# Kernel optimization log

Measured on AMD Instinct MI355X. Metric: run time of the kernel, lower is better.

Reference implementation:

```python
import jax, jax.numpy as jnp
import numpy as np

N_NODES = 50000
N_EDGES = 800000
IN_FEATS = 256
HIDDEN = 128
OUT_FEATS = 64


def setup_inputs() -> dict:
    key = jax.random.key(0)
    k1, k2, k3, k4, k5 = jax.random.split(key, 5)
    x = jax.random.normal(k1, (N_NODES, IN_FEATS), dtype=jnp.float32)
    src = jax.random.randint(k2, (N_EDGES,), 0, N_NODES, dtype=jnp.int64)
    dst = jax.random.randint(k3, (N_EDGES,), 0, N_NODES, dtype=jnp.int64)
    # Glorot-ish init for linear weights (DGL GraphConv uses xavier_uniform)
    W1 = jax.random.normal(k4, (IN_FEATS, HIDDEN), dtype=jnp.float32) / np.sqrt(IN_FEATS)
    W2 = jax.random.normal(k5, (HIDDEN, OUT_FEATS), dtype=jnp.float32) / np.sqrt(HIDDEN)
    b1 = jnp.zeros((HIDDEN,), dtype=jnp.float32)
    b2 = jnp.zeros((OUT_FEATS,), dtype=jnp.float32)
    return {"x": x, "src": src, "dst": dst, "W1": W1, "b1": b1, "W2": W2, "b2": b2}


def _norms(src, dst, n_nodes):
    ones = jnp.ones(src.shape[0], dtype=jnp.float32)
    deg_out = jax.ops.segment_sum(ones, src, num_segments=n_nodes)
    deg_in = jax.ops.segment_sum(ones, dst, num_segments=n_nodes)
    # DGL clamps zero degrees to 1 to avoid inf
    norm_src = jnp.power(jnp.clip(deg_out, 1.0, None), -0.5)  # [N]
    norm_dst = jnp.power(jnp.clip(deg_in, 1.0, None), -0.5)   # [N]
    return norm_src, norm_dst


def _gcn_layer(h, W, b, src, dst, norm_src, norm_dst, n_nodes):
    # norm='both': D_dst^{-1/2} A D_src^{-1/2} (h W) + b
    # multiply by W first (in_feats >= out_feats -> cheaper aggregation)
    m = (h * norm_src[:, None]) @ W            # [N, out]
    agg = jax.ops.segment_sum(m[src], dst, num_segments=n_nodes)  # [N, out]
    return agg * norm_dst[:, None] + b


def reference(x, src, dst, W1, b1, W2, b2):
    n = x.shape[0]
    norm_src, norm_dst = _norms(src, dst, n)
    h = _gcn_layer(x, W1, b1, src, dst, norm_src, norm_dst, n)
    h = jax.nn.relu(h)
    h = _gcn_layer(h, W2, b2, src, dst, norm_src, norm_dst, n)
    return h
```

## Files before the change

kernel.cpp:

```cpp
#include <hip/hip_runtime.h>

#define N_NODES 50000
#define N_EDGES 800000
#define IN_FEATS 256
#define HIDDEN 128
#define OUT_FEATS 64

#define NB 16384
#define NRANGE 4
#define NBT (NRANGE * NB)
#define NCHUNK 64
#define EPC 12500

typedef _Float16 f16;
typedef _Float16 f16x8 __attribute__((ext_vector_type(8)));
typedef float f32x4 __attribute__((ext_vector_type(4)));

__global__ __launch_bounds__(256) void hist_kernel(
    const int* __restrict__ src, const int* __restrict__ dst,
    unsigned* __restrict__ hist_src, unsigned* __restrict__ hist_dst) {
  __shared__ unsigned ls[NB / 2];
  __shared__ unsigned ld2[NB / 2];
  const int r = blockIdx.x % NRANGE;
  const int c = blockIdx.x / NRANGE;
  const int lo = r * NB;
  for (int i = threadIdx.x; i < NB / 2; i += 256) {
    ls[i] = 0;
    ld2[i] = 0;
  }
  __syncthreads();
  const int4* s4 = (const int4*)(src + c * EPC);
  const int4* d4 = (const int4*)(dst + c * EPC);
  for (int i = threadIdx.x; i < EPC / 4; i += 256) {
    int4 s = s4[i];
    int4 d = d4[i];
    unsigned b;
    b = (unsigned)(s.x - lo); if (b < NB) atomicAdd(&ls[b >> 1], 1u << ((b & 1) << 4));
    b = (unsigned)(s.y - lo); if (b < NB) atomicAdd(&ls[b >> 1], 1u << ((b & 1) << 4));
    b = (unsigned)(s.z - lo); if (b < NB) atomicAdd(&ls[b >> 1], 1u << ((b & 1) << 4));
    b = (unsigned)(s.w - lo); if (b < NB) atomicAdd(&ls[b >> 1], 1u << ((b & 1) << 4));
    b = (unsigned)(d.x - lo); if (b < NB) atomicAdd(&ld2[b >> 1], 1u << ((b & 1) << 4));
    b = (unsigned)(d.y - lo); if (b < NB) atomicAdd(&ld2[b >> 1], 1u << ((b & 1) << 4));
    b = (unsigned)(d.z - lo); if (b < NB) atomicAdd(&ld2[b >> 1], 1u << ((b & 1) << 4));
    b = (unsigned)(d.w - lo); if (b < NB) atomicAdd(&ld2[b >> 1], 1u << ((b & 1) << 4));
  }
  __syncthreads();
  unsigned* hs = hist_src + ((long)c * NBT + lo) / 2;
  unsigned* hd = hist_dst + ((long)c * NBT + lo) / 2;
  for (int i = threadIdx.x; i < NB / 2; i += 256) {
    hs[i] = ls[i];
    hd[i] = ld2[i];
  }
}

__global__ __launch_bounds__(256) void reduce_kernel(
    const unsigned* __restrict__ hist_src, unsigned* __restrict__ hist_dst,
    int* __restrict__ deg_in, float* __restrict__ norm_src,
    float* __restrict__ norm_dst, int* __restrict__ partial) {
  const unsigned short* hs = (const unsigned short*)hist_src;
  unsigned short* hd = (unsigned short*)hist_dst;
  int n = blockIdx.x * 256 + threadIdx.x;
  int run = 0;
  if (n < N_NODES) {
    int so = 0;
#pragma unroll 8
    for (int c = 0; c < NCHUNK; ++c) so += hs[(long)c * NBT + n];
    norm_src[n] = rsqrtf((float)max(so, 1));
#pragma unroll 8
    for (int c = 0; c < NCHUNK; ++c) {
      int t = hd[(long)c * NBT + n];
      hd[(long)c * NBT + n] = (unsigned short)run;
      run += t;
    }
    deg_in[n] = run;
    norm_dst[n] = rsqrtf((float)max(run, 1));
  }
  __shared__ int sd[256];
  sd[threadIdx.x] = run;
  __syncthreads();
  for (int s = 128; s > 0; s >>= 1) {
    if (threadIdx.x < s) sd[threadIdx.x] += sd[threadIdx.x + s];
    __syncthreads();
  }
  if (threadIdx.x == 0) partial[blockIdx.x] = sd[0];
}

__global__ __launch_bounds__(256) void scan2(int* __restrict__ partial,
                                             int nb) {
  __shared__ int sd[256];
  int v = (threadIdx.x < nb) ? partial[threadIdx.x] : 0;
  sd[threadIdx.x] = v;
  __syncthreads();
  for (int off = 1; off < 256; off <<= 1) {
    int t = sd[threadIdx.x] +
            ((threadIdx.x >= off) ? sd[threadIdx.x - off] : 0);
    __syncthreads();
    sd[threadIdx.x] = t;
    __syncthreads();
  }
  if (threadIdx.x < nb) partial[threadIdx.x] = sd[threadIdx.x] - v;
}

__global__ __launch_bounds__(256) void scan3(const int* __restrict__ deg,
                                             const int* __restrict__ partial,
                                             int* __restrict__ rowptr) {
  __shared__ int sd[256];
  int i = blockIdx.x * 256 + threadIdx.x;
  int v = (i < N_NODES) ? deg[i] : 0;
  sd[threadIdx.x] = v;
  __syncthreads();
  for (int off = 1; off < 256; off <<= 1) {
    int t = sd[threadIdx.x] +
            ((threadIdx.x >= off) ? sd[threadIdx.x - off] : 0);
    __syncthreads();
    sd[threadIdx.x] = t;
    __syncthreads();
  }
  if (i < N_NODES) rowptr[i] = partial[blockIdx.x] + sd[threadIdx.x] - v;
  if (blockIdx.x == 0 && threadIdx.x == 0) rowptr[N_NODES] = N_EDGES;
}

__global__ __launch_bounds__(256) void fill_csr(
    const int* __restrict__ src, const int* __restrict__ dst,
    const int* __restrict__ rowptr, const unsigned* __restrict__ pref32,
    int* __restrict__ col) {
  __shared__ int cur[NB];
  const unsigned short* pref = (const unsigned short*)pref32;
  const int r = blockIdx.x % NRANGE;
  const int c = blockIdx.x / NRANGE;
  const int lo = r * NB;
  for (int i = threadIdx.x; i < NB; i += 256) {
    int n = lo + i;
    cur[i] = (n < N_NODES) ? rowptr[n] + pref[(long)c * NBT + n] : 0;
  }
  __syncthreads();
  const int4* s4 = (const int4*)(src + c * EPC);
  const int4* d4 = (const int4*)(dst + c * EPC);
  for (int i = threadIdx.x; i < EPC / 4; i += 256) {
    int4 s = s4[i];
    int4 d = d4[i];
    unsigned b;
    b = (unsigned)(d.x - lo);
    if (b < NB) col[atomicAdd(&cur[b], 1)] = s.x;
    b = (unsigned)(d.y - lo);
    if (b < NB) col[atomicAdd(&cur[b], 1)] = s.y;
    b = (unsigned)(d.z - lo);
    if (b < NB) col[atomicAdd(&cur[b], 1)] = s.z;
    b = (unsigned)(d.w - lo);
    if (b < NB) col[atomicAdd(&cur[b], 1)] = s.w;
  }
}

__global__ __launch_bounds__(256) void wtrans(const float* __restrict__ W1,
                                              const float* __restrict__ W2,
                                              f16* __restrict__ W1T,
                                              f16* __restrict__ W2T) {
  int i = blockIdx.x * 256 + threadIdx.x;
  if (i < 128 * 256) {
    int n = i >> 8, k = i & 255;
    W1T[i] = (f16)W1[k * 128 + n];
  } else if (i < 128 * 256 + 64 * 128) {
    int j = i - 128 * 256;
    int n = j >> 7, k = j & 127;
    W2T[j] = (f16)W2[k * 64 + n];
  }
}

template <int K, int NC, int TN, bool FP32IN>
__global__ __launch_bounds__(256) void gemm_mfma(
    const void* __restrict__ Xv, const f16* __restrict__ WT,
    const float* __restrict__ ns, f16* __restrict__ Mout) {
  constexpr int KI = K / 32;
  constexpr int COLBLK = NC / (TN * 16);
  constexpr int KP = K + 8;
  __shared__ f16 Bs[TN * 16 * KP];

  const int cb = blockIdx.x % COLBLK;
  const int rb = blockIdx.x / COLBLK;
  const int col0 = cb * TN * 16;
  const int wave = threadIdx.x >> 6;
  const int lane = threadIdx.x & 63;
  const int m = lane & 15;
  const int q = lane >> 4;
  const int row0 = rb * 64 + wave * 16;

  for (int idx = threadIdx.x; idx < TN * 16 * (K / 8); idx += 256) {
    int n = idx / (K / 8);
    int kk = idx % (K / 8);
    *(f16x8*)(Bs + n * KP + kk * 8) =
        *(const f16x8*)(WT + (long)(col0 + n) * K + kk * 8);
  }
  __syncthreads();

  const int ra = min(row0 + m, N_NODES - 1);
  const float s = FP32IN ? ns[ra] : 0.f;

  f32x4 acc[TN];
#pragma unroll
  for (int t = 0; t < TN; ++t) acc[t] = (f32x4){0.f, 0.f, 0.f, 0.f};

#pragma unroll
  for (int ki = 0; ki < KI; ++ki) {
    const int kb = ki * 32 + q * 8;
    f16x8 a;
    if (FP32IN) {
      const float* X = (const float*)Xv;
      const float* p = X + (long)ra * K + kb;
      float4 u0 = *(const float4*)p;
      float4 u1 = *(const float4*)(p + 4);
      a[0] = (f16)(u0.x * s); a[1] = (f16)(u0.y * s);
      a[2] = (f16)(u0.z * s); a[3] = (f16)(u0.w * s);
      a[4] = (f16)(u1.x * s); a[5] = (f16)(u1.y * s);
      a[6] = (f16)(u1.z * s); a[7] = (f16)(u1.w * s);
    } else {
      const f16* X = (const f16*)Xv;
      a = *(const f16x8*)(X + (long)ra * K + kb);
    }
#pragma unroll
    for (int t = 0; t < TN; ++t) {
      f16x8 b = *(const f16x8*)(Bs + (t * 16 + m) * KP + kb);
      acc[t] = __builtin_amdgcn_mfma_f32_16x16x32_f16(a, b, acc[t], 0, 0, 0);
    }
  }

#pragma unroll
  for (int r = 0; r < 4; ++r) {
    int row = row0 + q * 4 + r;
    if (row < N_NODES) {
#pragma unroll
      for (int t = 0; t < TN; ++t)
        Mout[(long)row * NC + col0 + t * 16 + m] = (f16)acc[t][r];
    }
  }
}

__global__ __launch_bounds__(256) void gather1_kernel(
    const f16* __restrict__ M, const int* __restrict__ rowptr,
    const int* __restrict__ col, const float* __restrict__ nd,
    const float* __restrict__ ns, const float* __restrict__ b,
    f16* __restrict__ out) {
  constexpr int LPR = 16;
  constexpr int EPW = 64 / LPR;
  const int wave = threadIdx.x >> 6;
  const int lane = threadIdx.x & 63;
  const int eg = lane / LPR;
  const int t = lane % LPR;
  const int n = blockIdx.x * 4 + wave;
  if (n >= N_NODES) return;
  const int beg = rowptr[n];
  const int end = rowptr[n + 1];

  float acc[8];
#pragma unroll
  for (int j = 0; j < 8; ++j) acc[j] = 0.f;

  int i = beg + eg;
  for (; i + EPW < end; i += 2 * EPW) {
    int s0 = col[i];
    int s1 = col[i + EPW];
    f16x8 v0 = *(const f16x8*)(M + (long)s0 * HIDDEN + t * 8);
    f16x8 v1 = *(const f16x8*)(M + (long)s1 * HIDDEN + t * 8);
#pragma unroll
    for (int j = 0; j < 8; ++j) acc[j] += (float)v0[j] + (float)v1[j];
  }
  if (i < end) {
    int s0 = col[i];
    f16x8 v0 = *(const f16x8*)(M + (long)s0 * HIDDEN + t * 8);
#pragma unroll
    for (int j = 0; j < 8; ++j) acc[j] += (float)v0[j];
  }

#pragma unroll
  for (int m2 = LPR; m2 < 64; m2 <<= 1)
#pragma unroll
    for (int j = 0; j < 8; ++j) acc[j] += __shfl_xor(acc[j], m2, 64);

  if (eg == 0) {
    float s = nd[n];
    float sn = ns[n];
    float4 bb0 = *(const float4*)(b + t * 8);
    float4 bb1 = *(const float4*)(b + t * 8 + 4);
    f16x8 o;
    o[0] = (f16)(fmaxf(acc[0] * s + bb0.x, 0.f) * sn);
    o[1] = (f16)(fmaxf(acc[1] * s + bb0.y, 0.f) * sn);
    o[2] = (f16)(fmaxf(acc[2] * s + bb0.z, 0.f) * sn);
    o[3] = (f16)(fmaxf(acc[3] * s + bb0.w, 0.f) * sn);
    o[4] = (f16)(fmaxf(acc[4] * s + bb1.x, 0.f) * sn);
    o[5] = (f16)(fmaxf(acc[5] * s + bb1.y, 0.f) * sn);
    o[6] = (f16)(fmaxf(acc[6] * s + bb1.z, 0.f) * sn);
    o[7] = (f16)(fmaxf(acc[7] * s + bb1.w, 0.f) * sn);
    *(f16x8*)(out + (long)n * HIDDEN + t * 8) = o;
  }
}

__global__ __launch_bounds__(256) void gather2_kernel(
    const f16* __restrict__ M, const int* __restrict__ rowptr,
    const int* __restrict__ col, const float* __restrict__ nd,
    const float* __restrict__ b, float* __restrict__ out) {
  constexpr int LPR = 8;
  constexpr int EPW = 64 / LPR;
  const int wave = threadIdx.x >> 6;
  const int lane = threadIdx.x & 63;
  const int eg = lane / LPR;
  const int t = lane % LPR;
  const int n = blockIdx.x * 4 + wave;
  if (n >= N_NODES) return;
  const int beg = rowptr[n];
  const int end = rowptr[n + 1];

  float acc[8];
#pragma unroll
  for (int j = 0; j < 8; ++j) acc[j] = 0.f;

  int i = beg + eg;
  for (; i + EPW < end; i += 2 * EPW) {
    int s0 = col[i];
    int s1 = col[i + EPW];
    f16x8 v0 = *(const f16x8*)(M + (long)s0 * OUT_FEATS + t * 8);
    f16x8 v1 = *(const f16x8*)(M + (long)s1 * OUT_FEATS + t * 8);
#pragma unroll
    for (int j = 0; j < 8; ++j) acc[j] += (float)v0[j] + (float)v1[j];
  }
  if (i < end) {
    int s0 = col[i];
    f16x8 v0 = *(const f16x8*)(M + (long)s0 * OUT_FEATS + t * 8);
#pragma unroll
    for (int j = 0; j < 8; ++j) acc[j] += (float)v0[j];
  }

#pragma unroll
  for (int m2 = LPR; m2 < 64; m2 <<= 1)
#pragma unroll
    for (int j = 0; j < 8; ++j) acc[j] += __shfl_xor(acc[j], m2, 64);

  if (eg == 0) {
    float s = nd[n];
    float4 bb0 = *(const float4*)(b + t * 8);
    float4 bb1 = *(const float4*)(b + t * 8 + 4);
    float4 o0, o1;
    o0.x = acc[0] * s + bb0.x;
    o0.y = acc[1] * s + bb0.y;
    o0.z = acc[2] * s + bb0.z;
    o0.w = acc[3] * s + bb0.w;
    o1.x = acc[4] * s + bb1.x;
    o1.y = acc[5] * s + bb1.y;
    o1.z = acc[6] * s + bb1.z;
    o1.w = acc[7] * s + bb1.w;
    *(float4*)(out + (long)n * OUT_FEATS + t * 8) = o0;
    *(float4*)(out + (long)n * OUT_FEATS + t * 8 + 4) = o1;
  }
}

extern "C" void kernel_launch(void* const* d_in, const int* in_sizes, int n_in,
                              void* d_out, int out_size, void* d_ws,
                              size_t ws_size, hipStream_t stream) {
  const float* x = (const float*)d_in[0];
  const int* src = (const int*)d_in[1];
  const int* dst = (const int*)d_in[2];
  const float* W1 = (const float*)d_in[3];
  const float* b1 = (const float*)d_in[4];
  const float* W2 = (const float*)d_in[5];
  const float* b2 = (const float*)d_in[6];
  float* out = (float*)d_out;

  int* wi = (int*)d_ws;
  int* partial = wi;
  int* rowptr = wi + 256;
  int* deg_in = wi + 50260;
  int* col = wi + 100260;
  float* wf = (float*)d_ws + 900260;
  float* norm_src = wf;
  float* norm_dst = wf + 50000;
  f16* fh = (f16*)(wf + 100000);
  f16* W1T = fh;
  f16* W2T = fh + 128 * 256;
  f16* m1 = fh + 128 * 256 + 64 * 128;
  f16* h1p = m1 + (long)50048 * 128;
  f16* m2 = h1p + (long)50048 * 128;

  unsigned* hist_src = (unsigned*)m1;
  unsigned* hist_dst = hist_src + (long)NCHUNK * NBT / 2;

  const int nb_nodes = (N_NODES + 255) / 256;
  const int rowblk = (N_NODES + 63) / 64;

  hist_kernel<<<NRANGE * NCHUNK, 256, 0, stream>>>(src, dst, hist_src,
                                                   hist_dst);
  reduce_kernel<<<nb_nodes, 256, 0, stream>>>(hist_src, hist_dst, deg_in,
                                              norm_src, norm_dst, partial);
  scan2<<<1, 256, 0, stream>>>(partial, nb_nodes);
  scan3<<<nb_nodes, 256, 0, stream>>>(deg_in, partial, rowptr);
  fill_csr<<<NRANGE * NCHUNK, 256, 0, stream>>>(src, dst, rowptr, hist_dst,
                                                col);
  wtrans<<<(128 * 256 + 64 * 128 + 255) / 256, 256, 0, stream>>>(W1, W2, W1T,
                                                                 W2T);

  gemm_mfma<IN_FEATS, HIDDEN, 4, true>
      <<<rowblk * 2, 256, 0, stream>>>(x, W1T, norm_src, m1);
  gather1_kernel<<<(N_NODES + 3) / 4, 256, 0, stream>>>(m1, rowptr, col,
                                                        norm_dst, norm_src, b1,
                                                        h1p);

  gemm_mfma<HIDDEN, OUT_FEATS, 4, false>
      <<<rowblk, 256, 0, stream>>>(h1p, W2T, norm_src, m2);
  gather2_kernel<<<(N_NODES + 3) / 4, 256, 0, stream>>>(m2, rowptr, col,
                                                        norm_dst, b2, out);
}
```

Before: 241.5 us.

## Fuse CSR-building prep kernels into one cooperative kernel with grid syncs

Merges the histogram, degree reduction, two scan stages, CSR fill and weight transpose into a single cooperative kernel of 256 blocks separated by grid-wide barriers. This removes five kernel launches and their inter-kernel gaps from the preprocessing chain. In exchange, later phases run on a fixed 256-block grid with loops over work items, and each grid.sync adds barrier cost. The 64KB shared array may limit occupancy but must fit for the cooperative launch to succeed.

```diff
diff --git a/kernel.cpp b/kernel.cpp
--- a/kernel.cpp
+++ b/kernel.cpp
@@ -1,4 +1,7 @@
 #include <hip/hip_runtime.h>
+#include <hip/hip_cooperative_groups.h>
+
+namespace cg = cooperative_groups;
 
 #define N_NODES 50000
 #define N_EDGES 800000
@@ -16,153 +19,163 @@
 typedef _Float16 f16x8 __attribute__((ext_vector_type(8)));
 typedef float f32x4 __attribute__((ext_vector_type(4)));
 
-__global__ __launch_bounds__(256) void hist_kernel(
+__global__ __launch_bounds__(256) void prep_kernel(
     const int* __restrict__ src, const int* __restrict__ dst,
-    unsigned* __restrict__ hist_src, unsigned* __restrict__ hist_dst) {
-  __shared__ unsigned ls[NB / 2];
-  __shared__ unsigned ld2[NB / 2];
-  const int r = blockIdx.x % NRANGE;
-  const int c = blockIdx.x / NRANGE;
-  const int lo = r * NB;
-  for (int i = threadIdx.x; i < NB / 2; i += 256) {
-    ls[i] = 0;
-    ld2[i] = 0;
-  }
-  __syncthreads();
-  const int4* s4 = (const int4*)(src + c * EPC);
-  const int4* d4 = (const int4*)(dst + c * EPC);
-  for (int i = threadIdx.x; i < EPC / 4; i += 256) {
-    int4 s = s4[i];
-    int4 d = d4[i];
-    unsigned b;
-    b = (unsigned)(s.x - lo); if (b < NB) atomicAdd(&ls[b >> 1], 1u << ((b & 1) << 4));
-    b = (unsigned)(s.y - lo); if (b < NB) atomicAdd(&ls[b >> 1], 1u << ((b & 1) << 4));
-    b = (unsigned)(s.z - lo); if (b < NB) atomicAdd(&ls[b >> 1], 1u << ((b & 1) << 4));
-    b = (unsigned)(s.w - lo); if (b < NB) atomicAdd(&ls[b >> 1], 1u << ((b & 1) << 4));
-    b = (unsigned)(d.x - lo); if (b < NB) atomicAdd(&ld2[b >> 1], 1u << ((b & 1) << 4));
-    b = (unsigned)(d.y - lo); if (b < NB) atomicAdd(&ld2[b >> 1], 1u << ((b & 1) << 4));
-    b = (unsigned)(d.z - lo); if (b < NB) atomicAdd(&ld2[b >> 1], 1u << ((b & 1) << 4));
-    b = (unsigned)(d.w - lo); if (b < NB) atomicAdd(&ld2[b >> 1], 1u << ((b & 1) << 4));
-  }
-  __syncthreads();
-  unsigned* hs = hist_src + ((long)c * NBT + lo) / 2;
-  unsigned* hd = hist_dst + ((long)c * NBT + lo) / 2;
-  for (int i = threadIdx.x; i < NB / 2; i += 256) {
-    hs[i] = ls[i];
-    hd[i] = ld2[i];
-  }
-}
-
-__global__ __launch_bounds__(256) void reduce_kernel(
-    const unsigned* __restrict__ hist_src, unsigned* __restrict__ hist_dst,
+    const float* __restrict__ W1, const float* __restrict__ W2,
+    unsigned* __restrict__ hist_src, unsigned* __restrict__ hist_dst,
     int* __restrict__ deg_in, float* __restrict__ norm_src,
-    float* __restrict__ norm_dst, int* __restrict__ partial) {
-  const unsigned short* hs = (const unsigned short*)hist_src;
-  unsigned short* hd = (unsigned short*)hist_dst;
-  int n = blockIdx.x * 256 + threadIdx.x;
-  int run = 0;
-  if (n < N_NODES) {
-    int so = 0;
+    float* __restrict__ norm_dst, int* __restrict__ partial,
+    int* __restrict__ rowptr, int* __restrict__ col,
+    f16* __restrict__ W1T, f16* __restrict__ W2T) {
+  cg::grid_group grid = cg::this_grid();
+  __shared__ int lds[NB];
+  const int bid = blockIdx.x;
+  const int tid = threadIdx.x;
+
+  {
+    unsigned* ls = (unsigned*)lds;
+    unsigned* ld2 = (unsigned*)lds + NB / 2;
+    const int r = bid % NRANGE;
+    const int c = bid / NRANGE;
+    const int lo = r * NB;
+    for (int i = tid; i < NB / 2; i += 256) {
+      ls[i] = 0;
+      ld2[i] = 0;
+    }
+    __syncthreads();
+    const int4* s4 = (const int4*)(src + c * EPC);
+    const int4* d4 = (const int4*)(dst + c * EPC);
+    for (int i = tid; i < EPC / 4; i += 256) {
+      int4 s = s4[i];
+      int4 d = d4[i];
+      unsigned b;
+      b = (unsigned)(s.x - lo); if (b < NB) atomicAdd(&ls[b >> 1], 1u << ((b & 1) << 4));
+      b = (unsigned)(s.y - lo); if (b < NB) atomicAdd(&ls[b >> 1], 1u << ((b & 1) << 4));
+      b = (unsigned)(s.z - lo); if (b < NB) atomicAdd(&ls[b >> 1], 1u << ((b & 1) << 4));
+      b = (unsigned)(s.w - lo); if (b < NB) atomicAdd(&ls[b >> 1], 1u << ((b & 1) << 4));
+      b = (unsigned)(d.x - lo); if (b < NB) atomicAdd(&ld2[b >> 1], 1u << ((b & 1) << 4));
+      b = (unsigned)(d.y - lo); if (b < NB) atomicAdd(&ld2[b >> 1], 1u << ((b & 1) << 4));
+      b = (unsigned)(d.z - lo); if (b < NB) atomicAdd(&ld2[b >> 1], 1u << ((b & 1) << 4));
+      b = (unsigned)(d.w - lo); if (b < NB) atomicAdd(&ld2[b >> 1], 1u << ((b & 1) << 4));
+    }
+    __syncthreads();
+    unsigned* hs = hist_src + ((long)c * NBT + lo) / 2;
+    unsigned* hd = hist_dst + ((long)c * NBT + lo) / 2;
+    for (int i = tid; i < NB / 2; i += 256) {
+      hs[i] = ls[i];
+      hd[i] = ld2[i];
+    }
+  }
+  grid.sync();
+
+  {
+    const unsigned short* hs = (const unsigned short*)hist_src;
+    unsigned short* hd = (unsigned short*)hist_dst;
+    int* sd = lds;
+    for (int w = bid; w < 196 + 160; w += 256) {
+      if (w < 196) {
+        int n = w * 256 + tid;
+        int run = 0;
+        if (n < N_NODES) {
+          int so = 0;
 #pragma unroll 8
-    for (int c = 0; c < NCHUNK; ++c) so += hs[(long)c * NBT + n];
-    norm_src[n] = rsqrtf((float)max(so, 1));
+          for (int c = 0; c < NCHUNK; ++c) so += hs[(long)c * NBT + n];
+          norm_src[n] = rsqrtf((float)max(so, 1));
 #pragma unroll 8
-    for (int c = 0; c < NCHUNK; ++c) {
-      int t = hd[(long)c * NBT + n];
-      hd[(long)c * NBT + n] = (unsigned short)run;
-      run += t;
-    }
-    deg_in[n] = run;
-    norm_dst[n] = rsqrtf((float)max(run, 1));
-  }
-  __shared__ int sd[256];
-  sd[threadIdx.x] = run;
-  __syncthreads();
-  for (int s = 128; s > 0; s >>= 1) {
-    if (threadIdx.x < s) sd[threadIdx.x] += sd[threadIdx.x + s];
+          for (int c = 0; c < NCHUNK; ++c) {
+            int t = hd[(long)c * NBT + n];
+            hd[(long)c * NBT + n] = (unsigned short)run;
+            run += t;
+          }
+          deg_in[n] = run;
+          norm_dst[n] = rsqrtf((float)max(run, 1));
+        }
+        __syncthreads();
+        sd[tid] = run;
+        __syncthreads();
+        for (int s = 128; s > 0; s >>= 1) {
+          if (tid < s) sd[tid] += sd[tid + s];
+          __syncthreads();
+        }
+        if (tid == 0) partial[w] = sd[0];
+        __syncthreads();
+      } else {
+        int i = (w - 196) * 256 + tid;
+        if (i < 128 * 256) {
+          int n = i >> 8, k = i & 255;
+          W1T[i] = (f16)W1[k * 128 + n];
+        } else {
+          int j = i - 128 * 256;
+          int n = j >> 7, k = j & 127;
+          W2T[j] = (f16)W2[k * 64 + n];
+        }
+      }
+    }
+  }
+  grid.sync();
+
+  if (bid == 0) {
+    int* sd = lds;
+    int v = (tid < 196) ? partial[tid] : 0;
+    sd[tid] = v;
     __syncthreads();
-  }
-  if (threadIdx.x == 0) partial[blockIdx.x] = sd[0];
-}
-
-__global__ __launch_bounds__(256) void scan2(int* __restrict__ partial,
-                                             int nb) {
-  __shared__ int sd[256];
-  int v = (threadIdx.x < nb) ? partial[threadIdx.x] : 0;
-  sd[threadIdx.x] = v;
-  __syncthreads();
-  for (int off = 1; off < 256; off <<= 1) {
-    int t = sd[threadIdx.x] +
-            ((threadIdx.x >= off) ? sd[threadIdx.x - off] : 0);
+    for (int off = 1; off < 256; off <<= 1) {
+      int t = sd[tid] + ((tid >= off) ? sd[tid - off] : 0);
+      __syncthreads();
+      sd[tid] = t;
+      __syncthreads();
+    }
+    if (tid < 196) partial[tid] = sd[tid] - v;
+  }
+  grid.sync();
+
+  {
+    int* sd = lds;
+    for (int w = bid; w < 196; w += 256) {
+      int i = w * 256 + tid;
+      int v = (i < N_NODES) ? deg_in[i] : 0;
+      __syncthreads();
+      sd[tid] = v;
+      __syncthreads();
+      for (int off = 1; off < 256; off <<= 1) {
+        int t = sd[tid] + ((tid >= off) ? sd[tid - off] : 0);
+        __syncthreads();
+        sd[tid] = t;
+        __syncthreads();
+      }
+      if (i < N_NODES) rowptr[i] = partial[w] + sd[tid] - v;
+      if (w == 0 && tid == 0) rowptr[N_NODES] = N_EDGES;
+      __syncthreads();
+    }
+  }
+  grid.sync();
+
+  {
+    int* cur = lds;
+    const unsigned short* pref = (const unsigned short*)hist_dst;
+    const int r = bid % NRANGE;
+    const int c = bid / NRANGE;
+    const int lo = r * NB;
+    for (int i = tid; i < NB; i += 256) {
+      int n = lo + i;
+      cur[i] = (n < N_NODES) ? rowptr[n] + pref[(long)c * NBT + n] : 0;
+    }
     __syncthreads();
-    sd[threadIdx.x] = t;
-    __syncthreads();
-  }
-  if (threadIdx.x < nb) partial[threadIdx.x] = sd[threadIdx.x] - v;
-}
-
-__global__ __launch_bounds__(256) void scan3(const int* __restrict__ deg,
-                                             const int* __restrict__ partial,
-                                             int* __restrict__ rowptr) {
-  __shared__ int sd[256];
-  int i = blockIdx.x * 256 + threadIdx.x;
-  int v = (i < N_NODES) ? deg[i] : 0;
-  sd[threadIdx.x] = v;
-  __syncthreads();
-  for (int off = 1; off < 256; off <<= 1) {
-    int t = sd[threadIdx.x] +
-            ((threadIdx.x >= off) ? sd[threadIdx.x - off] : 0);
-    __syncthreads();
-    sd[threadIdx.x] = t;
-    __syncthreads();
-  }
-  if (i < N_NODES) rowptr[i] = partial[blockIdx.x] + sd[threadIdx.x] - v;
-  if (blockIdx.x == 0 && threadIdx.x == 0) rowptr[N_NODES] = N_EDGES;
-}
-
-__global__ __launch_bounds__(256) void fill_csr(
-    const int* __restrict__ src, const int* __restrict__ dst,
-    const int* __restrict__ rowptr, const unsigned* __restrict__ pref32,
-    int* __restrict__ col) {
-  __shared__ int cur[NB];
-  const unsigned short* pref = (const unsigned short*)pref32;
-  const int r = blockIdx.x % NRANGE;
-  const int c = blockIdx.x / NRANGE;
-  const int lo = r * NB;
-  for (int i = threadIdx.x; i < NB; i += 256) {
-    int n = lo + i;
-    cur[i] = (n < N_NODES) ? rowptr[n] + pref[(long)c * NBT + n] : 0;
-  }
-  __syncthreads();
-  const int4* s4 = (const int4*)(src + c * EPC);
-  const int4* d4 = (const int4*)(dst + c * EPC);
-  for (int i = threadIdx.x; i < EPC / 4; i += 256) {
-    int4 s = s4[i];
-    int4 d = d4[i];
-    unsigned b;
-    b = (unsigned)(d.x - lo);
-    if (b < NB) col[atomicAdd(&cur[b], 1)] = s.x;
-    b = (unsigned)(d.y - lo);
-    if (b < NB) col[atomicAdd(&cur[b], 1)] = s.y;
-    b = (unsigned)(d.z - lo);
-    if (b < NB) col[atomicAdd(&cur[b], 1)] = s.z;
-    b = (unsigned)(d.w - lo);
-    if (b < NB) col[atomicAdd(&cur[b], 1)] = s.w;
-  }
-}
-
-__global__ __launch_bounds__(256) void wtrans(const float* __restrict__ W1,
-                                              const float* __restrict__ W2,
-                                              f16* __restrict__ W1T,
-                                              f16* __restrict__ W2T) {
-  int i = blockIdx.x * 256 + threadIdx.x;
-  if (i < 128 * 256) {
-    int n = i >> 8, k = i & 255;
-    W1T[i] = (f16)W1[k * 128 + n];
-  } else if (i < 128 * 256 + 64 * 128) {
-    int j = i - 128 * 256;
-    int n = j >> 7, k = j & 127;
-    W2T[j] = (f16)W2[k * 64 + n];
+    const int4* s4 = (const int4*)(src + c * EPC);
+    const int4* d4 = (const int4*)(dst + c * EPC);
+    for (int i = tid; i < EPC / 4; i += 256) {
+      int4 s = s4[i];
+      int4 d = d4[i];
+      unsigned b;
+      b = (unsigned)(d.x - lo);
+      if (b < NB) col[atomicAdd(&cur[b], 1)] = s.x;
+      b = (unsigned)(d.y - lo);
+      if (b < NB) col[atomicAdd(&cur[b], 1)] = s.y;
+      b = (unsigned)(d.z - lo);
+      if (b < NB) col[atomicAdd(&cur[b], 1)] = s.z;
+      b = (unsigned)(d.w - lo);
+      if (b < NB) col[atomicAdd(&cur[b], 1)] = s.w;
+    }
   }
 }
 
@@ -381,19 +394,15 @@
   unsigned* hist_src = (unsigned*)m1;
   unsigned* hist_dst = hist_src + (long)NCHUNK * NBT / 2;
 
-  const int nb_nodes = (N_NODES + 255) / 256;
   const int rowblk = (N_NODES + 63) / 64;
 
-  hist_kernel<<<NRANGE * NCHUNK, 256, 0, stream>>>(src, dst, hist_src,
-                                                   hist_dst);
-  reduce_kernel<<<nb_nodes, 256, 0, stream>>>(hist_src, hist_dst, deg_in,
-                                              norm_src, norm_dst, partial);
-  scan2<<<1, 256, 0, stream>>>(partial, nb_nodes);
-  scan3<<<nb_nodes, 256, 0, stream>>>(deg_in, partial, rowptr);
-  fill_csr<<<NRANGE * NCHUNK, 256, 0, stream>>>(src, dst, rowptr, hist_dst,
-                                                col);
-  wtrans<<<(128 * 256 + 64 * 128 + 255) / 256, 256, 0, stream>>>(W1, W2, W1T,
-                                                                 W2T);
+  void* args[] = {(void*)&src,      (void*)&dst,      (void*)&W1,
+                  (void*)&W2,       (void*)&hist_src, (void*)&hist_dst,
+                  (void*)&deg_in,   (void*)&norm_src, (void*)&norm_dst,
+                  (void*)&partial,  (void*)&rowptr,   (void*)&col,
+                  (void*)&W1T,      (void*)&W2T};
+  hipLaunchCooperativeKernel((void*)prep_kernel, dim3(NRANGE * NCHUNK),
+                             dim3(256), args, 0, stream);
 
   gemm_mfma<IN_FEATS, HIDDEN, 4, true>
       <<<rowblk * 2, 256, 0, stream>>>(x, W1T, norm_src, m1);
```

After: 370.5 us. +53.5%, slower.
